# Optimization experiments

Measured on AMD Instinct MI355X. Metric: run time of the kernel, lower is better.

Reference implementation:

```python
import jax, jax.numpy as jnp
import numpy as np

N_NODES = 100_000
N_EDGES = 3_200_000
N_FEAT = 128
N_HID = 8
N_CLASSES = 10


def setup_inputs() -> dict:
    key = jax.random.key(0)
    ks = jax.random.split(key, 16)
    g = lambda k, shape, fan_in: jax.random.normal(k, shape, jnp.float32) / np.sqrt(fan_in)
    inp = {}
    inp['x'] = jax.random.normal(ks[0], (N_NODES, N_FEAT), jnp.float32)
    inp['edge_index'] = jax.random.randint(ks[1], (2, N_EDGES), 0, N_NODES, jnp.int32)
    # lin: Linear(F, 8)
    inp['lin_w'] = g(ks[2], (N_FEAT, N_HID), N_FEAT)
    inp['lin_b'] = jnp.zeros((N_HID,), jnp.float32)
    # conv1: GATConv(8, 8, heads=2)
    inp['w1'] = g(ks[3], (N_HID, 2 * N_HID), N_HID)
    inp['a1_src'] = g(ks[4], (2, N_HID), N_HID)
    inp['a1_dst'] = g(ks[5], (2, N_HID), N_HID)
    inp['b1'] = jnp.zeros((2 * N_HID,), jnp.float32)
    # conv2: GATConv(16, 8, heads=2)
    inp['w2'] = g(ks[6], (2 * N_HID, 2 * N_HID), 2 * N_HID)
    inp['a2_src'] = g(ks[7], (2, N_HID), N_HID)
    inp['a2_dst'] = g(ks[8], (2, N_HID), N_HID)
    inp['b2'] = jnp.zeros((2 * N_HID,), jnp.float32)
    # conv3: GATConv(16, num_classes, heads=1, concat=False)
    inp['w3'] = g(ks[9], (2 * N_HID, N_CLASSES), 2 * N_HID)
    inp['a3_src'] = g(ks[10], (1, N_CLASSES), N_CLASSES)
    inp['a3_dst'] = g(ks[11], (1, N_CLASSES), N_CLASSES)
    inp['b3'] = jnp.zeros((N_CLASSES,), jnp.float32)
    return inp


def _gat_conv(x, W, a_src, a_dst, b, src, dst, heads, out_c, concat):
    """PyG GATConv with pre-appended self-loops in (src, dst)."""
    N = x.shape[0]
    xl = (x @ W).reshape(N, heads, out_c)                 # [N,H,C]
    alpha_src = (xl * a_src[None]).sum(-1)                # [N,H]
    alpha_dst = (xl * a_dst[None]).sum(-1)                # [N,H]
    e = jax.nn.leaky_relu(alpha_src[src] + alpha_dst[dst], 0.2)  # [E,H]
    # segment softmax over destination nodes
    m = jax.ops.segment_max(e, dst, num_segments=N)
    e = jnp.exp(e - m[dst])
    s = jax.ops.segment_sum(e, dst, num_segments=N)
    alpha = e / s[dst]                                    # [E,H]
    msg = xl[src] * alpha[:, :, None]                     # [E,H,C]
    out = jax.ops.segment_sum(msg, dst, num_segments=N)   # [N,H,C]
    out = out.reshape(N, heads * out_c) if concat else out.mean(axis=1)
    return out + b


def reference(x, edge_index, lin_w, lin_b, w1, a1_src, a1_dst, b1,
              w2, a2_src, a2_dst, b2, w3, a3_src, a3_dst, b3):
    N = x.shape[0]
    loops = jnp.arange(N, dtype=edge_index.dtype)
    src = jnp.concatenate([edge_index[0], loops])
    dst = jnp.concatenate([edge_index[1], loops])
    lrelu = lambda v: jax.nn.leaky_relu(v, 0.01)
    h = lrelu(x @ lin_w + lin_b)
    h = lrelu(_gat_conv(h, w1, a1_src, a1_dst, b1, src, dst, 2, N_HID, True))
    h = lrelu(_gat_conv(h, w2, a2_src, a2_dst, b2, src, dst, 2, N_HID, True))
    h = _gat_conv(h, w3, a3_src, a3_dst, b3, src, dst, 1, N_CLASSES, False)
    return jax.nn.log_softmax(h, axis=-1)
```

## Files before the change

kernel.cpp:

```cpp
#include <hip/hip_runtime.h>
#include <hip/hip_fp16.h>
#include <math.h>

#define N_NODES 100000
#define N_EDGES 3200000
#define ET (N_EDGES + N_NODES)
#define SLOT 80
#define KMAX 5
#define SHIFT 8
#define BNODES 256
#define NBUCK 391
#define BCAP 9088
#define P1_T 1024
#define E_PER 16
#define P1_WG ((N_EDGES + P1_T * E_PER - 1) / (P1_T * E_PER))
#define SCAN_T 1024
#define SCAN_CHUNK 98

__device__ __forceinline__ float lrelu(float v, float s) { return v > 0.f ? v : v * s; }

__global__ __launch_bounds__(256) void lin_kernel(const float* __restrict__ x,
                                                  const float* __restrict__ w,
                                                  const float* __restrict__ b,
                                                  float* __restrict__ h0) {
    int lane = threadIdx.x & 63;
    int wid = blockIdx.x * 4 + (threadIdx.x >> 6);
    float4 wa0 = *(const float4*)&w[lane * 8];
    float4 wa1 = *(const float4*)&w[lane * 8 + 4];
    float4 wb0 = *(const float4*)&w[(lane + 64) * 8];
    float4 wb1 = *(const float4*)&w[(lane + 64) * 8 + 4];
    float wk0[8] = {wa0.x, wa0.y, wa0.z, wa0.w, wa1.x, wa1.y, wa1.z, wa1.w};
    float wk1[8] = {wb0.x, wb0.y, wb0.z, wb0.w, wb1.x, wb1.y, wb1.z, wb1.w};
    int l = lane & 7;
    int kmap = 4 * (l & 1) + 2 * ((l >> 1) & 1) + ((l >> 2) & 1);
    float bk = b[kmap];
#pragma unroll
    for (int j = 0; j < 4; j++) {
        int n = wid * 4 + j;
        if (n >= N_NODES) break;
        float x0 = x[n * 128 + lane];
        float x1 = x[n * 128 + 64 + lane];
        float acc[8];
#pragma unroll
        for (int k = 0; k < 8; k++) acc[k] = x0 * wk0[k] + x1 * wk1[k];
#pragma unroll
        for (int k = 0; k < 4; k++) {
            float keep = (lane & 1) ? acc[k + 4] : acc[k];
            float give = (lane & 1) ? acc[k] : acc[k + 4];
            acc[k] = keep + __shfl_xor(give, 1, 64);
        }
#pragma unroll
        for (int k = 0; k < 2; k++) {
            float keep = (lane & 2) ? acc[k + 2] : acc[k];
            float give = (lane & 2) ? acc[k] : acc[k + 2];
            acc[k] = keep + __shfl_xor(give, 2, 64);
        }
        {
            float keep = (lane & 4) ? acc[1] : acc[0];
            float give = (lane & 4) ? acc[0] : acc[1];
            acc[0] = keep + __shfl_xor(give, 4, 64);
        }
        acc[0] += __shfl_xor(acc[0], 8, 64);
        acc[0] += __shfl_xor(acc[0], 16, 64);
        acc[0] += __shfl_xor(acc[0], 32, 64);
        if (lane < 8) h0[n * 8 + kmap] = lrelu(acc[0] + bk, 0.01f);
    }
}

__global__ void __launch_bounds__(P1_T) part_kernel(const int* __restrict__ ei,
                                                    int* __restrict__ bcur,
                                                    unsigned* __restrict__ pairs) {
    __shared__ int hist[NBUCK];
    __shared__ int gbase[NBUCK];
    int t = threadIdx.x;
    for (int i = t; i < NBUCK; i += P1_T) hist[i] = 0;
    __syncthreads();
    int base = blockIdx.x * (P1_T * E_PER);
    int s[E_PER], d[E_PER], r[E_PER];
#pragma unroll
    for (int k = 0; k < E_PER; k++) {
        int e = base + k * P1_T + t;
        if (e < N_EDGES) {
            s[k] = ei[e];
            d[k] = ei[N_EDGES + e];
            r[k] = atomicAdd(&hist[d[k] >> SHIFT], 1);
        }
    }
    __syncthreads();
    for (int i = t; i < NBUCK; i += P1_T)
        gbase[i] = (hist[i] > 0) ? atomicAdd(&bcur[i], hist[i]) : 0;
    __syncthreads();
#pragma unroll
    for (int k = 0; k < E_PER; k++) {
        int e = base + k * P1_T + t;
        if (e < N_EDGES) {
            int b = d[k] >> SHIFT;
            int pos = gbase[b] + r[k];
            if (pos < BCAP)
                pairs[(size_t)b * BCAP + pos] =
                    ((unsigned)(d[k] & (BNODES - 1)) << 17) | (unsigned)s[k];
        }
    }
}

__global__ void build_kernel(const int* __restrict__ bcur, const unsigned* __restrict__ pairs,
                             int* __restrict__ csr, int* __restrict__ deg) {
    __shared__ int offs[BNODES];
    int b = blockIdx.x;
    int t = threadIdx.x;
    int node0 = b << SHIFT;
    int n = node0 + t;
    if (n < N_NODES) {
        csr[n * SLOT] = n;
        offs[t] = 1;
    } else offs[t] = 0;
    __syncthreads();
    int cnt = min(bcur[b], BCAP);
    for (int i = t; i < cnt; i += BNODES) {
        unsigned v = pairs[(size_t)b * BCAP + i];
        int ln = v >> 17;
        int s = v & 0x1FFFF;
        int pos = atomicAdd(&offs[ln], 1);
        if (pos < SLOT) csr[(node0 + ln) * SLOT + pos] = s;
    }
    __syncthreads();
    if (n < N_NODES) deg[n] = offs[t];
}

__global__ void count_kernel(const int* __restrict__ ei, int* __restrict__ deg) {
    int e = blockIdx.x * blockDim.x + threadIdx.x;
    if (e >= ET) return;
    int d = (e < N_EDGES) ? ei[N_EDGES + e] : (e - N_EDGES);
    atomicAdd(&deg[d], 1);
}

__global__ void scan_kernel(const int* __restrict__ deg, int* __restrict__ rowptr,
                            int* __restrict__ cursor) {
    __shared__ int sums[SCAN_T];
    int t = threadIdx.x;
    int start = t * SCAN_CHUNK;
    int end = min(start + SCAN_CHUNK, N_NODES);
    int s = 0;
    for (int i = start; i < end; i++) s += deg[i];
    sums[t] = s;
    __syncthreads();
    for (int off = 1; off < SCAN_T; off <<= 1) {
        int v = sums[t];
        int add = (t >= off) ? sums[t - off] : 0;
        __syncthreads();
        sums[t] = v + add;
        __syncthreads();
    }
    int base = (t > 0) ? sums[t - 1] : 0;
    for (int i = start; i < end; i++) {
        rowptr[i] = base;
        cursor[i] = base;
        base += deg[i];
    }
    if (t == SCAN_T - 1) rowptr[N_NODES] = base;
}

__global__ void scatter_kernel(const int* __restrict__ ei, int* __restrict__ cursor,
                               int* __restrict__ csr) {
    int e = blockIdx.x * blockDim.x + threadIdx.x;
    if (e >= ET) return;
    int s, d;
    if (e < N_EDGES) { s = ei[e]; d = ei[N_EDGES + e]; } else { s = d = e - N_EDGES; }
    int pos = atomicAdd(&cursor[d], 1);
    csr[pos] = s;
}

template <int CIN, int H, int C, int XLS>
__global__ void prep_kernel(const float* __restrict__ hin, const float* __restrict__ W,
                            const float* __restrict__ a_src, const float* __restrict__ a_dst,
                            __half* __restrict__ xl, float* __restrict__ asrc,
                            float* __restrict__ adst) {
    __shared__ float Ws[CIN * H * C];
    __shared__ float As[H * C];
    __shared__ float Ad[H * C];
    for (int i = threadIdx.x; i < CIN * H * C; i += blockDim.x) Ws[i] = W[i];
    for (int i = threadIdx.x; i < H * C; i += blockDim.x) { As[i] = a_src[i]; Ad[i] = a_dst[i]; }
    __syncthreads();
    int n = blockIdx.x * blockDim.x + threadIdx.x;
    if (n >= N_NODES) return;
    float hreg[CIN];
#pragma unroll
    for (int i = 0; i < CIN; i += 4) {
        float4 v = *(const float4*)&hin[n * CIN + i];
        hreg[i] = v.x; hreg[i + 1] = v.y; hreg[i + 2] = v.z; hreg[i + 3] = v.w;
    }
#pragma unroll
    for (int h = 0; h < H; h++) {
        float as = 0.f, ad = 0.f;
#pragma unroll
        for (int c = 0; c < C; c++) {
            float v = 0.f;
#pragma unroll
            for (int i = 0; i < CIN; i++) v += hreg[i] * Ws[i * H * C + h * C + c];
            xl[n * XLS + h * C + c] = __float2half_rn(v);
            as += v * As[h * C + c];
            ad += v * Ad[h * C + c];
        }
        asrc[n * H + h] = as;
        adst[n * H + h] = ad;
    }
#pragma unroll
    for (int c = H * C; c < XLS; c++) xl[n * XLS + c] = __float2half_rn(0.f);
}

__global__ void gat64_h2(const int* __restrict__ cnt_, const int* __restrict__ csr,
                         const float* __restrict__ asrc, const float* __restrict__ adst,
                         const __half* __restrict__ xl, const float* __restrict__ b,
                         float* __restrict__ hout) {
    int n = blockIdx.x * 4 + (threadIdx.x >> 6);
    int lane = threadIdx.x & 63;
    int eg = lane >> 2;
    int cp = lane & 3;
    int h = cp >> 1;
    if (n >= N_NODES) return;
    int beg = n * SLOT;
    int cnt = min(cnt_[n], SLOT);
    float adn = adst[n * 2 + h];
    int idx[KMAX];
#pragma unroll
    for (int k = 0; k < KMAX; k++) {
        int i = eg + (k << 4);
        idx[k] = (i < cnt) ? csr[beg + i] : -1;
    }
    float ssum = 0.f, pa0 = 0.f, pa1 = 0.f, pa2 = 0.f, pa3 = 0.f;
#pragma unroll
    for (int k = 0; k < KMAX; k++) {
        int s = idx[k];
        if (s >= 0) {
            float e = asrc[s * 2 + h] + adn;
            float w = __expf(fmaxf(e, 0.2f * e));
            float2 raw = *(const float2*)&xl[s * 16 + 4 * cp];
            __half2 x01 = *(__half2*)&raw.x;
            __half2 x23 = *(__half2*)&raw.y;
            float2 f01 = __half22float2(x01);
            float2 f23 = __half22float2(x23);
            ssum += w;
            pa0 += w * f01.x; pa1 += w * f01.y;
            pa2 += w * f23.x; pa3 += w * f23.y;
        }
    }
    ssum += __shfl_xor(ssum, 4, 64); ssum += __shfl_xor(ssum, 8, 64);
    ssum += __shfl_xor(ssum, 16, 64); ssum += __shfl_xor(ssum, 32, 64);
    float q0, q1;
    {
        float k0 = (lane & 4) ? pa2 : pa0, g0 = (lane & 4) ? pa0 : pa2;
        float k1 = (lane & 4) ? pa3 : pa1, g1 = (lane & 4) ? pa1 : pa3;
        q0 = k0 + __shfl_xor(g0, 4, 64);
        q1 = k1 + __shfl_xor(g1, 4, 64);
    }
    float v;
    {
        float k0 = (lane & 8) ? q1 : q0, g0 = (lane & 8) ? q0 : q1;
        v = k0 + __shfl_xor(g0, 8, 64);
    }
    v += __shfl_xor(v, 16, 64);
    v += __shfl_xor(v, 32, 64);
    if (lane < 16) {
        int ch = 4 * (lane & 3) + 2 * ((lane >> 2) & 1) + ((lane >> 3) & 1);
        hout[n * 16 + ch] = lrelu(v / ssum + b[ch], 0.01f);
    }
}

__global__ void gat64_ls(const int* __restrict__ cnt_, const int* __restrict__ csr,
                         const float* __restrict__ asrc, const float* __restrict__ adst,
                         const __half* __restrict__ xl, const float* __restrict__ b,
                         float* __restrict__ out) {
    int n = blockIdx.x * 4 + (threadIdx.x >> 6);
    int lane = threadIdx.x & 63;
    int eg = lane >> 2;
    int cp = lane & 3;
    if (n >= N_NODES) return;
    int beg = n * SLOT;
    int cnt = min(cnt_[n], SLOT);
    float adn = adst[n];
    int idx[KMAX];
#pragma unroll
    for (int k = 0; k < KMAX; k++) {
        int i = eg + (k << 4);
        idx[k] = (i < cnt) ? csr[beg + i] : -1;
    }
    float ssum = 0.f, pa0 = 0.f, pa1 = 0.f, pa2 = 0.f, pa3 = 0.f;
#pragma unroll
    for (int k = 0; k < KMAX; k++) {
        int s = idx[k];
        if (s >= 0) {
            float e = asrc[s] + adn;
            float w = __expf(fmaxf(e, 0.2f * e));
            float2 raw = *(const float2*)&xl[s * 16 + 4 * cp];
            __half2 x01 = *(__half2*)&raw.x;
            __half2 x23 = *(__half2*)&raw.y;
            float2 f01 = __half22float2(x01);
            float2 f23 = __half22float2(x23);
            ssum += w;
            pa0 += w * f01.x; pa1 += w * f01.y;
            pa2 += w * f23.x; pa3 += w * f23.y;
        }
    }
    ssum += __shfl_xor(ssum, 4, 64); ssum += __shfl_xor(ssum, 8, 64);
    ssum += __shfl_xor(ssum, 16, 64); ssum += __shfl_xor(ssum, 32, 64);
    float q0, q1;
    {
        float k0 = (lane & 4) ? pa2 : pa0, g0 = (lane & 4) ? pa0 : pa2;
        float k1 = (lane & 4) ? pa3 : pa1, g1 = (lane & 4) ? pa1 : pa3;
        q0 = k0 + __shfl_xor(g0, 4, 64);
        q1 = k1 + __shfl_xor(g1, 4, 64);
    }
    float pv;
    {
        float k0 = (lane & 8) ? q1 : q0, g0 = (lane & 8) ? q0 : q1;
        pv = k0 + __shfl_xor(g0, 8, 64);
    }
    pv += __shfl_xor(pv, 16, 64);
    pv += __shfl_xor(pv, 32, 64);
    int ch = 4 * (lane & 3) + 2 * ((lane >> 2) & 1) + ((lane >> 3) & 1);
    float v = (ch < 10) ? pv / ssum + b[ch] : -INFINITY;
    float vm = v;
#pragma unroll
    for (int off = 8; off >= 1; off >>= 1) vm = fmaxf(vm, __shfl_xor(vm, off, 16));
    float ex = (ch < 10) ? __expf(v - vm) : 0.f;
#pragma unroll
    for (int off = 8; off >= 1; off >>= 1) ex += __shfl_xor(ex, off, 16);
    float lse = vm + __logf(ex);
    if (lane < 16 && ch < 10) out[n * 10 + ch] = v - lse;
}

__global__ void gat16_h2(const int* __restrict__ rowptr, const int* __restrict__ csr,
                         const float* __restrict__ asrc, const float* __restrict__ adst,
                         const __half* __restrict__ xl, const float* __restrict__ b,
                         float* __restrict__ hout) {
    int tid = blockIdx.x * blockDim.x + threadIdx.x;
    int wave = tid >> 6;
    int lane = threadIdx.x & 63;
    int g = lane >> 4;
    int c = lane & 15;
    int h = c >> 3;
    int n = wave * 4 + g;
    if (n >= N_NODES) return;
    int beg = rowptr[n], cnt = rowptr[n + 1] - beg;
    float adn = adst[n * 2 + h];
    float ssum = 0.f, pa = 0.f;
#pragma unroll 4
    for (int i = 0; i < cnt; i++) {
        int s = csr[beg + i];
        float e = asrc[s * 2 + h] + adn;
        float w = __expf(fmaxf(e, 0.2f * e));
        ssum += w;
        pa += w * __half2float(xl[s * 16 + c]);
    }
    hout[n * 16 + c] = lrelu(pa / ssum + b[c], 0.01f);
}

__global__ void gat16_ls(const int* __restrict__ rowptr, const int* __restrict__ csr,
                         const float* __restrict__ asrc, const float* __restrict__ adst,
                         const __half* __restrict__ xl, const float* __restrict__ b,
                         float* __restrict__ out) {
    int tid = blockIdx.x * blockDim.x + threadIdx.x;
    int wave = tid >> 6;
    int lane = threadIdx.x & 63;
    int g = lane >> 4;
    int c = lane & 15;
    int n = wave * 4 + g;
    if (n >= N_NODES) return;
    int beg = rowptr[n], cnt = rowptr[n + 1] - beg;
    float adn = adst[n];
    float ssum = 0.f, pa = 0.f;
#pragma unroll 4
    for (int i = 0; i < cnt; i++) {
        int s = csr[beg + i];
        float e = asrc[s] + adn;
        float w = __expf(fmaxf(e, 0.2f * e));
        ssum += w;
        pa += w * __half2float(xl[s * 16 + c]);
    }
    float v = pa / ssum + ((c < 10) ? b[c] : 0.f);
    float vm = (c < 10) ? v : -INFINITY;
#pragma unroll
    for (int off = 8; off >= 1; off >>= 1) vm = fmaxf(vm, __shfl_xor(vm, off, 16));
    float ex = (c < 10) ? __expf(v - vm) : 0.f;
    float sum = ex;
#pragma unroll
    for (int off = 8; off >= 1; off >>= 1) sum += __shfl_xor(sum, off, 16);
    float lse = vm + __logf(sum);
    if (c < 10) out[n * 10 + c] = v - lse;
}

extern "C" void kernel_launch(void* const* d_in, const int* in_sizes, int n_in,
                              void* d_out, int out_size, void* d_ws, size_t ws_size,
                              hipStream_t stream) {
    const float* x     = (const float*)d_in[0];
    const int*   ei    = (const int*)d_in[1];
    const float* lin_w = (const float*)d_in[2];
    const float* lin_b = (const float*)d_in[3];
    const float* w1    = (const float*)d_in[4];
    const float* a1s   = (const float*)d_in[5];
    const float* a1d   = (const float*)d_in[6];
    const float* b1    = (const float*)d_in[7];
    const float* w2    = (const float*)d_in[8];
    const float* a2s   = (const float*)d_in[9];
    const float* a2d   = (const float*)d_in[10];
    const float* b2    = (const float*)d_in[11];
    const float* w3    = (const float*)d_in[12];
    const float* a3s   = (const float*)d_in[13];
    const float* a3d   = (const float*)d_in[14];
    const float* b3    = (const float*)d_in[15];

    float* ws = (float*)d_ws;
    float* slotH  = ws;
    __half* slotX = (__half*)(ws + 1600000);
    float* as_    = ws + 3200000;
    float* ad_    = ws + 3400000;
    unsigned* pairs = (unsigned*)ws;
    int* csrP = (int*)(ws + 3600000);
    int* degP = (int*)(ws + 3600000 + N_NODES * SLOT);
    int* bcur = degP + N_NODES;
    size_t need_new = (size_t)(3600000 + N_NODES * SLOT + N_NODES + 512) * 4;

    int use_bucket = (ws_size >= need_new) ? 1 : 0;

    int* degC    = (int*)(ws + 3600000);
    int* rowptrC = degC + N_NODES;
    int* cursorC = rowptrC + N_NODES + 1;
    int* csrC    = cursorC + N_NODES;

    dim3 B(256);
    int nb_n  = (N_NODES + 255) / 256;
    int nb_et = (ET + 255) / 256;
    int nb_g  = (N_NODES + 15) / 16;
    int nb_w  = (N_NODES + 3) / 4;

    if (use_bucket) {
        hipMemsetAsync(bcur, 0, 512 * sizeof(int), stream);
        part_kernel<<<P1_WG, P1_T, 0, stream>>>(ei, bcur, pairs);
        build_kernel<<<NBUCK, BNODES, 0, stream>>>(bcur, pairs, csrP, degP);
    } else {
        hipMemsetAsync(degC, 0, N_NODES * sizeof(int), stream);
        count_kernel<<<nb_et, B, 0, stream>>>(ei, degC);
        scan_kernel<<<1, SCAN_T, 0, stream>>>(degC, rowptrC, cursorC);
        scatter_kernel<<<nb_et, B, 0, stream>>>(ei, cursorC, csrC);
    }

    lin_kernel<<<dim3((N_NODES + 15) / 16), B, 0, stream>>>(x, lin_w, lin_b, slotH);

    prep_kernel<8, 2, 8, 16><<<nb_n, B, 0, stream>>>(slotH, w1, a1s, a1d, slotX, as_, ad_);
    if (use_bucket) gat64_h2<<<nb_w, B, 0, stream>>>(degP, csrP, as_, ad_, slotX, b1, slotH);
    else            gat16_h2<<<nb_g, B, 0, stream>>>(rowptrC, csrC, as_, ad_, slotX, b1, slotH);

    prep_kernel<16, 2, 8, 16><<<nb_n, B, 0, stream>>>(slotH, w2, a2s, a2d, slotX, as_, ad_);
    if (use_bucket) gat64_h2<<<nb_w, B, 0, stream>>>(degP, csrP, as_, ad_, slotX, b2, slotH);
    else            gat16_h2<<<nb_g, B, 0, stream>>>(rowptrC, csrC, as_, ad_, slotX, b2, slotH);

    prep_kernel<16, 1, 10, 16><<<nb_n, B, 0, stream>>>(slotH, w3, a3s, a3d, slotX, as_, ad_);
    if (use_bucket) gat64_ls<<<nb_w, B, 0, stream>>>(degP, csrP, as_, ad_, slotX, b3, (float*)d_out);
    else            gat16_ls<<<nb_g, B, 0, stream>>>(rowptrC, csrC, as_, ad_, slotX, b3, (float*)d_out);
}
```

Baseline: 332.3 us.

## Process two nodes per wave in bucketed GAT kernels with DPP reductions

Each wave in the bucketed GAT aggregation kernels now handles two destination nodes instead of one. The lane mapping is rearranged so the channel pair sits in the high lane bits, which lets the first reduction steps use DPP quad permutes instead of cross-lane shuffles. The grid is halved to match, giving more independent gathers in flight per wave and fewer reduction instructions per node. The gather loop also drops the bounds check on the node index, which relies on N_NODES being divisible by 8.

```diff
diff --git a/kernel.cpp b/kernel.cpp
--- a/kernel.cpp
+++ b/kernel.cpp
@@ -18,6 +18,28 @@
 #define SCAN_CHUNK 98
 
 __device__ __forceinline__ float lrelu(float v, float s) { return v > 0.f ? v : v * s; }
+
+template <int CTRL>
+__device__ __forceinline__ float dppmov(float v) {
+    return __int_as_float(__builtin_amdgcn_update_dpp(0, __float_as_int(v), CTRL, 0xF, 0xF, true));
+}
+
+__device__ __forceinline__ void reduce16(float& v, float& ssum, float pa0, float pa1,
+                                         float pa2, float pa3, int lane) {
+    int b0 = lane & 1, b1 = (lane >> 1) & 1;
+    float k0 = b0 ? pa2 : pa0, g0 = b0 ? pa0 : pa2;
+    float k1 = b0 ? pa3 : pa1, g1 = b0 ? pa1 : pa3;
+    float q0 = k0 + dppmov<0xB1>(g0);
+    float q1 = k1 + dppmov<0xB1>(g1);
+    float kk = b1 ? q1 : q0, gg = b1 ? q0 : q1;
+    v = kk + dppmov<0x4E>(gg);
+    v += __shfl_xor(v, 4, 64);
+    v += __shfl_xor(v, 8, 64);
+    ssum += dppmov<0xB1>(ssum);
+    ssum += dppmov<0x4E>(ssum);
+    ssum += __shfl_xor(ssum, 4, 64);
+    ssum += __shfl_xor(ssum, 8, 64);
+}
 
 __global__ __launch_bounds__(256) void lin_kernel(const float* __restrict__ x,
                                                   const float* __restrict__ w,
@@ -208,125 +230,138 @@
     for (int c = H * C; c < XLS; c++) xl[n * XLS + c] = __float2half_rn(0.f);
 }
 
-__global__ void gat64_h2(const int* __restrict__ cnt_, const int* __restrict__ csr,
-                         const float* __restrict__ asrc, const float* __restrict__ adst,
-                         const __half* __restrict__ xl, const float* __restrict__ b,
-                         float* __restrict__ hout) {
-    int n = blockIdx.x * 4 + (threadIdx.x >> 6);
+__global__ __launch_bounds__(256) void gat64_h2(const int* __restrict__ cnt_,
+                                                const int* __restrict__ csr,
+                                                const float* __restrict__ asrc,
+                                                const float* __restrict__ adst,
+                                                const __half* __restrict__ xl,
+                                                const float* __restrict__ b,
+                                                float* __restrict__ hout) {
+    int wg = blockIdx.x * 4 + (threadIdx.x >> 6);
     int lane = threadIdx.x & 63;
-    int eg = lane >> 2;
-    int cp = lane & 3;
+    int eg = lane & 15;
+    int cp = lane >> 4;
     int h = cp >> 1;
-    if (n >= N_NODES) return;
-    int beg = n * SLOT;
-    int cnt = min(cnt_[n], SLOT);
-    float adn = adst[n * 2 + h];
-    int idx[KMAX];
+    int n0 = wg * 2, n1 = n0 + 1;
+    int cnt0 = min(cnt_[n0], SLOT);
+    int cnt1 = min(cnt_[n1], SLOT);
+    float ad0 = adst[n0 * 2 + h];
+    float ad1 = adst[n1 * 2 + h];
+    int idx0[KMAX], idx1[KMAX];
 #pragma unroll
     for (int k = 0; k < KMAX; k++) {
         int i = eg + (k << 4);
-        idx[k] = (i < cnt) ? csr[beg + i] : -1;
-    }
-    float ssum = 0.f, pa0 = 0.f, pa1 = 0.f, pa2 = 0.f, pa3 = 0.f;
+        idx0[k] = (i < cnt0) ? csr[n0 * SLOT + i] : -1;
+        idx1[k] = (i < cnt1) ? csr[n1 * SLOT + i] : -1;
+    }
+    float s0 = 0.f, a00 = 0.f, a01 = 0.f, a02 = 0.f, a03 = 0.f;
+    float s1 = 0.f, a10 = 0.f, a11 = 0.f, a12 = 0.f, a13 = 0.f;
 #pragma unroll
     for (int k = 0; k < KMAX; k++) {
-        int s = idx[k];
+        int s = idx0[k];
         if (s >= 0) {
-            float e = asrc[s * 2 + h] + adn;
+            float e = asrc[s * 2 + h] + ad0;
             float w = __expf(fmaxf(e, 0.2f * e));
             float2 raw = *(const float2*)&xl[s * 16 + 4 * cp];
-            __half2 x01 = *(__half2*)&raw.x;
-            __half2 x23 = *(__half2*)&raw.y;
-            float2 f01 = __half22float2(x01);
-            float2 f23 = __half22float2(x23);
-            ssum += w;
-            pa0 += w * f01.x; pa1 += w * f01.y;
-            pa2 += w * f23.x; pa3 += w * f23.y;
-        }
-    }
-    ssum += __shfl_xor(ssum, 4, 64); ssum += __shfl_xor(ssum, 8, 64);
-    ssum += __shfl_xor(ssum, 16, 64); ssum += __shfl_xor(ssum, 32, 64);
-    float q0, q1;
-    {
-        float k0 = (lane & 4) ? pa2 : pa0, g0 = (lane & 4) ? pa0 : pa2;
-        float k1 = (lane & 4) ? pa3 : pa1, g1 = (lane & 4) ? pa1 : pa3;
-        q0 = k0 + __shfl_xor(g0, 4, 64);
-        q1 = k1 + __shfl_xor(g1, 4, 64);
-    }
-    float v;
-    {
-        float k0 = (lane & 8) ? q1 : q0, g0 = (lane & 8) ? q0 : q1;
-        v = k0 + __shfl_xor(g0, 8, 64);
-    }
-    v += __shfl_xor(v, 16, 64);
-    v += __shfl_xor(v, 32, 64);
-    if (lane < 16) {
-        int ch = 4 * (lane & 3) + 2 * ((lane >> 2) & 1) + ((lane >> 3) & 1);
-        hout[n * 16 + ch] = lrelu(v / ssum + b[ch], 0.01f);
-    }
-}
-
-__global__ void gat64_ls(const int* __restrict__ cnt_, const int* __restrict__ csr,
-                         const float* __restrict__ asrc, const float* __restrict__ adst,
-                         const __half* __restrict__ xl, const float* __restrict__ b,
-                         float* __restrict__ out) {
-    int n = blockIdx.x * 4 + (threadIdx.x >> 6);
+            float2 f01 = __half22float2(*(__half2*)&raw.x);
+            float2 f23 = __half22float2(*(__half2*)&raw.y);
+            s0 += w;
+            a00 += w * f01.x; a01 += w * f01.y; a02 += w * f23.x; a03 += w * f23.y;
+        }
+        int t = idx1[k];
+        if (t >= 0) {
+            float e = asrc[t * 2 + h] + ad1;
+            float w = __expf(fmaxf(e, 0.2f * e));
+            float2 raw = *(const float2*)&xl[t * 16 + 4 * cp];
+            float2 f01 = __half22float2(*(__half2*)&raw.x);
+            float2 f23 = __half22float2(*(__half2*)&raw.y);
+            s1 += w;
+            a10 += w * f01.x; a11 += w * f01.y; a12 += w * f23.x; a13 += w * f23.y;
+        }
+    }
+    float v0, v1;
+    reduce16(v0, s0, a00, a01, a02, a03, lane);
+    reduce16(v1, s1, a10, a11, a12, a13, lane);
+    if ((lane & 12) == 0) {
+        int ch = 4 * cp + 2 * (lane & 1) + ((lane >> 1) & 1);
+        float bc = b[ch];
+        hout[n0 * 16 + ch] = lrelu(v0 / s0 + bc, 0.01f);
+        hout[n1 * 16 + ch] = lrelu(v1 / s1 + bc, 0.01f);
+    }
+}
+
+__global__ __launch_bounds__(256) void gat64_ls(const int* __restrict__ cnt_,
+                                                const int* __restrict__ csr,
+                                                const float* __restrict__ asrc,
+                                                const float* __restrict__ adst,
+                                                const __half* __restrict__ xl,
+                                                const float* __restrict__ b,
+                                                float* __restrict__ out) {
+    int wg = blockIdx.x * 4 + (threadIdx.x >> 6);
     int lane = threadIdx.x & 63;
-    int eg = lane >> 2;
-    int cp = lane & 3;
-    if (n >= N_NODES) return;
-    int beg = n * SLOT;
-    int cnt = min(cnt_[n], SLOT);
-    float adn = adst[n];
-    int idx[KMAX];
+    int eg = lane & 15;
+    int cp = lane >> 4;
+    int n0 = wg * 2, n1 = n0 + 1;
+    int cnt0 = min(cnt_[n0], SLOT);
+    int cnt1 = min(cnt_[n1], SLOT);
+    float ad0 = adst[n0];
+    float ad1 = adst[n1];
+    int idx0[KMAX], idx1[KMAX];
 #pragma unroll
     for (int k = 0; k < KMAX; k++) {
         int i = eg + (k << 4);
-        idx[k] = (i < cnt) ? csr[beg + i] : -1;
-    }
-    float ssum = 0.f, pa0 = 0.f, pa1 = 0.f, pa2 = 0.f, pa3 = 0.f;
+        idx0[k] = (i < cnt0) ? csr[n0 * SLOT + i] : -1;
+        idx1[k] = (i < cnt1) ? csr[n1 * SLOT + i] : -1;
+    }
+    float s0 = 0.f, a00 = 0.f, a01 = 0.f, a02 = 0.f, a03 = 0.f;
+    float s1 = 0.f, a10 = 0.f, a11 = 0.f, a12 = 0.f, a13 = 0.f;
 #pragma unroll
     for (int k = 0; k < KMAX; k++) {
-        int s = idx[k];
+        int s = idx0[k];
         if (s >= 0) {
-            float e = asrc[s] + adn;
+            float e = asrc[s] + ad0;
             float w = __expf(fmaxf(e, 0.2f * e));
             float2 raw = *(const float2*)&xl[s * 16 + 4 * cp];
-            __half2 x01 = *(__half2*)&raw.x;
-            __half2 x23 = *(__half2*)&raw.y;
-            float2 f01 = __half22float2(x01);
-            float2 f23 = __half22float2(x23);
-            ssum += w;
-            pa0 += w * f01.x; pa1 += w * f01.y;
-            pa2 += w * f23.x; pa3 += w * f23.y;
-        }
-    }
-    ssum += __shfl_xor(ssum, 4, 64); ssum += __shfl_xor(ssum, 8, 64);
-    ssum += __shfl_xor(ssum, 16, 64); ssum += __shfl_xor(ssum, 32, 64);
-    float q0, q1;
-    {
-        float k0 = (lane & 4) ? pa2 : pa0, g0 = (lane & 4) ? pa0 : pa2;
-        float k1 = (lane & 4) ? pa3 : pa1, g1 = (lane & 4) ? pa1 : pa3;
-        q0 = k0 + __shfl_xor(g0, 4, 64);
-        q1 = k1 + __shfl_xor(g1, 4, 64);
-    }
-    float pv;
-    {
-        float k0 = (lane & 8) ? q1 : q0, g0 = (lane & 8) ? q0 : q1;
-        pv = k0 + __shfl_xor(g0, 8, 64);
-    }
-    pv += __shfl_xor(pv, 16, 64);
-    pv += __shfl_xor(pv, 32, 64);
-    int ch = 4 * (lane & 3) + 2 * ((lane >> 2) & 1) + ((lane >> 3) & 1);
-    float v = (ch < 10) ? pv / ssum + b[ch] : -INFINITY;
-    float vm = v;
-#pragma unroll
-    for (int off = 8; off >= 1; off >>= 1) vm = fmaxf(vm, __shfl_xor(vm, off, 16));
-    float ex = (ch < 10) ? __expf(v - vm) : 0.f;
-#pragma unroll
-    for (int off = 8; off >= 1; off >>= 1) ex += __shfl_xor(ex, off, 16);
-    float lse = vm + __logf(ex);
-    if (lane < 16 && ch < 10) out[n * 10 + ch] = v - lse;
+            float2 f01 = __half22float2(*(__half2*)&raw.x);
+            float2 f23 = __half22float2(*(__half2*)&raw.y);
+            s0 += w;
+            a00 += w * f01.x; a01 += w * f01.y; a02 += w * f23.x; a03 += w * f23.y;
+        }
+        int t = idx1[k];
+        if (t >= 0) {
+            float e = asrc[t] + ad1;
+            float w = __expf(fmaxf(e, 0.2f * e));
+            float2 raw = *(const float2*)&xl[t * 16 + 4 * cp];
+            float2 f01 = __half22float2(*(__half2*)&raw.x);
+            float2 f23 = __half22float2(*(__half2*)&raw.y);
+            s1 += w;
+            a10 += w * f01.x; a11 += w * f01.y; a12 += w * f23.x; a13 += w * f23.y;
+        }
+    }
+    float v0, v1;
+    reduce16(v0, s0, a00, a01, a02, a03, lane);
+    reduce16(v1, s1, a10, a11, a12, a13, lane);
+    int ch = 4 * cp + 2 * (lane & 1) + ((lane >> 1) & 1);
+    float bc = (ch < 10) ? b[ch] : 0.f;
+    float u0 = (ch < 10) ? v0 / s0 + bc : -INFINITY;
+    float u1 = (ch < 10) ? v1 / s1 + bc : -INFINITY;
+    float m0 = u0, m1 = u1;
+    m0 = fmaxf(m0, dppmov<0xB1>(m0)); m1 = fmaxf(m1, dppmov<0xB1>(m1));
+    m0 = fmaxf(m0, dppmov<0x4E>(m0)); m1 = fmaxf(m1, dppmov<0x4E>(m1));
+    m0 = fmaxf(m0, __shfl_xor(m0, 16, 64)); m1 = fmaxf(m1, __shfl_xor(m1, 16, 64));
+    m0 = fmaxf(m0, __shfl_xor(m0, 32, 64)); m1 = fmaxf(m1, __shfl_xor(m1, 32, 64));
+    float e0 = (ch < 10) ? __expf(u0 - m0) : 0.f;
+    float e1 = (ch < 10) ? __expf(u1 - m1) : 0.f;
+    e0 += dppmov<0xB1>(e0); e1 += dppmov<0xB1>(e1);
+    e0 += dppmov<0x4E>(e0); e1 += dppmov<0x4E>(e1);
+    e0 += __shfl_xor(e0, 16, 64); e1 += __shfl_xor(e1, 16, 64);
+    e0 += __shfl_xor(e0, 32, 64); e1 += __shfl_xor(e1, 32, 64);
+    float lse0 = m0 + __logf(e0);
+    float lse1 = m1 + __logf(e1);
+    if ((lane & 12) == 0 && ch < 10) {
+        out[n0 * 10 + ch] = u0 - lse0;
+        out[n1 * 10 + ch] = u1 - lse1;
+    }
 }
 
 __global__ void gat16_h2(const int* __restrict__ rowptr, const int* __restrict__ csr,
@@ -431,7 +466,7 @@
     int nb_n  = (N_NODES + 255) / 256;
     int nb_et = (ET + 255) / 256;
     int nb_g  = (N_NODES + 15) / 16;
-    int nb_w  = (N_NODES + 3) / 4;
+    int nb_w2 = N_NODES / 8;
 
     if (use_bucket) {
         hipMemsetAsync(bcur, 0, 512 * sizeof(int), stream);
@@ -447,14 +482,14 @@
     lin_kernel<<<dim3((N_NODES + 15) / 16), B, 0, stream>>>(x, lin_w, lin_b, slotH);
 
     prep_kernel<8, 2, 8, 16><<<nb_n, B, 0, stream>>>(slotH, w1, a1s, a1d, slotX, as_, ad_);
-    if (use_bucket) gat64_h2<<<nb_w, B, 0, stream>>>(degP, csrP, as_, ad_, slotX, b1, slotH);
+    if (use_bucket) gat64_h2<<<nb_w2, B, 0, stream>>>(degP, csrP, as_, ad_, slotX, b1, slotH);
     else            gat16_h2<<<nb_g, B, 0, stream>>>(rowptrC, csrC, as_, ad_, slotX, b1, slotH);
 
     prep_kernel<16, 2, 8, 16><<<nb_n, B, 0, stream>>>(slotH, w2, a2s, a2d, slotX, as_, ad_);
-    if (use_bucket) gat64_h2<<<nb_w, B, 0, stream>>>(degP, csrP, as_, ad_, slotX, b2, slotH);
+    if (use_bucket) gat64_h2<<<nb_w2, B, 0, stream>>>(degP, csrP, as_, ad_, slotX, b2, slotH);
     else            gat16_h2<<<nb_g, B, 0, stream>>>(rowptrC, csrC, as_, ad_, slotX, b2, slotH);
 
     prep_kernel<16, 1, 10, 16><<<nb_n, B, 0, stream>>>(slotH, w3, a3s, a3d, slotX, as_, ad_);
-    if (use_bucket) gat64_ls<<<nb_w, B, 0, stream>>>(degP, csrP, as_, ad_, slotX, b3, (float*)d_out);
+    if (use_bucket) gat64_ls<<<nb_w2, B, 0, stream>>>(degP, csrP, as_, ad_, slotX, b3, (float*)d_out);
     else            gat16_ls<<<nb_g, B, 0, stream>>>(rowptrC, csrC, as_, ad_, slotX, b3, (float*)d_out);
 }
```

Result: no change. 331.4 us (-0.3%).
